# Performance work log

Measured on AMD Instinct MI355X. Metric: run time of the kernel, lower is better.

The kernel has to match this reference:

```python
import jax, jax.numpy as jnp
from jax import lax
import numpy as np

T, B, X, Y = 24, 16, 32, 32
FS, FM, FC = 64, 16, 16
I = FS + FM + FC  # GRU input size = 96
H = 32            # hidden_size


def setup_inputs() -> dict:
    key = jax.random.key(0)
    ks = jax.random.split(key, 8)
    s = 1.0 / np.sqrt(H)  # pytorch GRU init scale
    return {
        "spatial": jax.random.normal(ks[0], (B, X, Y, FS), jnp.float32),
        "meteorology": jax.random.normal(ks[1], (T, B, X, Y, FM), jnp.float32),
        "context": jax.random.normal(ks[2], (T, B, X, Y, FC), jnp.float32),
        "W_ih": jax.random.uniform(ks[3], (3 * H, I), jnp.float32, -s, s),
        "W_hh": jax.random.uniform(ks[4], (3 * H, H), jnp.float32, -s, s),
        "b_ih": jax.random.uniform(ks[5], (3 * H,), jnp.float32, -s, s),
        "b_hh": jax.random.uniform(ks[6], (3 * H,), jnp.float32, -s, s),
        "W": jax.random.normal(ks[7], (H, FS), jnp.float32),
    }


def _gru_final_state(x, W_ih, W_hh, b_ih, b_hh):
    # x: (T, N, I); returns final hidden state (N, H). PyTorch GRU cell math.
    n_batch = x.shape[1]
    h0 = jnp.zeros((n_batch, H), x.dtype)

    def step(h, xt):
        gi = xt @ W_ih.T + b_ih          # (N, 3H)
        gh = h @ W_hh.T + b_hh           # (N, 3H)
        i_r, i_z, i_n = jnp.split(gi, 3, axis=-1)
        h_r, h_z, h_n = jnp.split(gh, 3, axis=-1)
        r = jax.nn.sigmoid(i_r + h_r)
        z = jax.nn.sigmoid(i_z + h_z)
        n = jnp.tanh(i_n + r * h_n)
        h_new = (1.0 - z) * n + z * h
        return h_new, None

    hT, _ = lax.scan(step, h0, x)
    return hT


def reference(spatial, meteorology, context, W_ih, W_hh, b_ih, b_hh, W):
    # Broadcast static spatial features over time and concat along feature dim.
    t = meteorology.shape[0]
    sp = jnp.broadcast_to(spatial[None], (t,) + spatial.shape)
    x = jnp.concatenate([sp, meteorology, context], axis=-1)  # (T,B,X,Y,I)
    # Batch all spatial positions into one recurrence: (T, B*X*Y, I)
    x = x.reshape(t, B * X * Y, I)
    hT = _gru_final_state(x, W_ih, W_hh, b_ih, b_hh)          # (B*X*Y, H)
    out = hT @ W                                              # (B*X*Y, FS)
    return out.reshape(B, X, Y, FS)
```

## Files before the change

kernel.cpp:

```cpp
#include <hip/hip_runtime.h>
#include <hip/hip_fp16.h>
#include <math.h>


typedef __attribute__((ext_vector_type(8))) _Float16 half8;
typedef __attribute__((ext_vector_type(4))) float f32x4;
typedef __attribute__((ext_vector_type(4))) unsigned int uix4;

#define NSEQ 16384
#define TSTEPS 24
#define LOG2E 1.44269504088896340736f

__device__ __forceinline__ float exp2_fast(float x) {
#if __has_builtin(__builtin_amdgcn_exp2f)
  return __builtin_amdgcn_exp2f(x);
#else
  return __expf(x * 0.6931471805599453f);
#endif
}

__device__ __forceinline__ unsigned int pk_f16(float a, float b) {
#if __has_builtin(__builtin_amdgcn_cvt_pkrtz)
  auto r = __builtin_amdgcn_cvt_pkrtz(a, b);
  return __builtin_bit_cast(unsigned int, r);
#else
  return (unsigned)__half_as_ushort(__float2half(a)) |
         ((unsigned)__half_as_ushort(__float2half(b)) << 16);
#endif
}
__device__ __forceinline__ unsigned int pk_f16_rn(float a, float b) {
  return (unsigned)__half_as_ushort(__float2half(a)) |
         ((unsigned)__half_as_ushort(__float2half(b)) << 16);
}
__device__ __forceinline__ half8 mk_h8(unsigned int a, unsigned int b,
                                       unsigned int c, unsigned int d) {
  uix4 v = {a, b, c, d};
  return __builtin_bit_cast(half8, v);
}
__device__ __forceinline__ f32x4 mfma_h(half8 a, half8 b, f32x4 c) {
  return __builtin_amdgcn_mfma_f32_16x16x32_f16(a, b, c, 0, 0, 0);
}

__device__ __forceinline__ void barrier_lds() {
  asm volatile("s_waitcnt lgkmcnt(0)" ::: "memory");
  __builtin_amdgcn_s_barrier();
}

__global__ __launch_bounds__(128, 4)
void gru10(const float* __restrict__ spatial,
           const float* __restrict__ met,
           const float* __restrict__ ctx,
           const float* __restrict__ W_ih,
           const float* __restrict__ W_hh,
           const float* __restrict__ b_ih,
           const float* __restrict__ b_hh,
           const float* __restrict__ Wp,
           float* __restrict__ out) {
  __shared__ float xls[2][6][16][20];

  const int tid = threadIdx.x;
  const int lane = tid & 63;
  const int wv = tid >> 6;
  const int l15 = lane & 15;
  const int c = lane >> 4;
  const int seq = blockIdx.x * 16 + l15;
  const f32x4 zero4 = {0.f, 0.f, 0.f, 0.f};

  if (wv == 1) {
    half8 wmc[6];
    f32x4 acc_i[6];
#pragma unroll
    for (int j = 0; j < 6; ++j) {
      const float sc = (j < 4) ? LOG2E : (2.0f * LOG2E);
      const float* mr = W_ih + (size_t)(j * 16 + l15) * 96 + 64 + c * 8;
      float4 wa = *(const float4*)mr;
      float4 wb = *(const float4*)(mr + 4);
      wmc[j] = mk_h8(pk_f16_rn(wa.x * sc, wa.y * sc),
                     pk_f16_rn(wa.z * sc, wa.w * sc),
                     pk_f16_rn(wb.x * sc, wb.y * sc),
                     pk_f16_rn(wb.z * sc, wb.w * sc));
      const int rowb = j * 16 + 4 * c;
      float4 vih = *(const float4*)(b_ih + rowb);
      if (j < 4) {
        float4 vhh = *(const float4*)(b_hh + rowb);
        acc_i[j][0] = (vih.x + vhh.x) * sc; acc_i[j][1] = (vih.y + vhh.y) * sc;
        acc_i[j][2] = (vih.z + vhh.z) * sc; acc_i[j][3] = (vih.w + vhh.w) * sc;
      } else {
        acc_i[j][0] = vih.x * sc; acc_i[j][1] = vih.y * sc;
        acc_i[j][2] = vih.z * sc; acc_i[j][3] = vih.w * sc;
      }
    }
#pragma unroll
    for (int kt = 0; kt < 2; ++kt) {
      const float* sp = spatial + (size_t)seq * 64 + kt * 32 + c * 8;
      float4 a0 = *(const float4*)sp;
      float4 a1 = *(const float4*)(sp + 4);
      half8 sf = mk_h8(pk_f16(a0.x, a0.y), pk_f16(a0.z, a0.w),
                       pk_f16(a1.x, a1.y), pk_f16(a1.z, a1.w));
#pragma unroll
      for (int j = 0; j < 6; ++j) {
        const float sc = (j < 4) ? LOG2E : (2.0f * LOG2E);
        const float* wr = W_ih + (size_t)(j * 16 + l15) * 96 + kt * 32 + c * 8;
        float4 wa = *(const float4*)wr;
        float4 wb = *(const float4*)(wr + 4);
        half8 wsp = mk_h8(pk_f16_rn(wa.x * sc, wa.y * sc),
                          pk_f16_rn(wa.z * sc, wa.w * sc),
                          pk_f16_rn(wb.x * sc, wb.y * sc),
                          pk_f16_rn(wb.z * sc, wb.w * sc));
        acc_i[j] = mfma_h(wsp, sf, acc_i[j]);
      }
    }
    const float* lptr = ((c < 2) ? met : ctx) + (size_t)seq * 16 + (c & 1) * 8;
    {
      float4 a0 = *(const float4*)lptr;
      float4 a1 = *(const float4*)(lptr + 4);
      half8 xf = mk_h8(pk_f16(a0.x, a0.y), pk_f16(a0.z, a0.w),
                       pk_f16(a1.x, a1.y), pk_f16(a1.z, a1.w));
#pragma unroll
      for (int j = 0; j < 6; ++j) {
        f32x4 D = mfma_h(wmc[j], xf, acc_i[j]);
        *(f32x4*)&xls[0][j][l15][c * 4] = D;
      }
    }
    float4 xs0a = *(const float4*)(lptr + (size_t)1 * NSEQ * 16);
    float4 xs0b = *(const float4*)(lptr + (size_t)1 * NSEQ * 16 + 4);
    float4 xs1a = *(const float4*)(lptr + (size_t)2 * NSEQ * 16);
    float4 xs1b = *(const float4*)(lptr + (size_t)2 * NSEQ * 16 + 4);

    barrier_lds();

#pragma unroll 2
    for (int t = 0; t < TSTEPS; ++t) {
      float4 xa = (t & 1) ? xs1a : xs0a;
      float4 xb = (t & 1) ? xs1b : xs0b;
      half8 xf = mk_h8(pk_f16(xa.x, xa.y), pk_f16(xa.z, xa.w),
                       pk_f16(xb.x, xb.y), pk_f16(xb.z, xb.w));
      {
        int tf = (t + 3 < TSTEPS) ? (t + 3) : (TSTEPS - 1);
        float4 na = *(const float4*)(lptr + (size_t)tf * NSEQ * 16);
        float4 nb = *(const float4*)(lptr + (size_t)tf * NSEQ * 16 + 4);
        if (t & 1) { xs1a = na; xs1b = nb; } else { xs0a = na; xs0b = nb; }
      }
      const int buf = (t + 1) & 1;
#pragma unroll
      for (int j = 0; j < 6; ++j) {
        f32x4 D = mfma_h(wmc[j], xf, acc_i[j]);
        *(f32x4*)&xls[buf][j][l15][c * 4] = D;
      }
      barrier_lds();
    }
  } else {
    __builtin_amdgcn_s_setprio(1);
    half8 whh[6];
#pragma unroll
    for (int j = 0; j < 6; ++j) {
      const float sc = (j < 4) ? LOG2E : (2.0f * LOG2E);
      const float* wr = W_hh + (size_t)(j * 16 + l15) * 32;
      float4 a = *(const float4*)(wr + 4 * c);
      float4 b = *(const float4*)(wr + 16 + 4 * c);
      whh[j] = mk_h8(pk_f16_rn(a.x * sc, a.y * sc),
                     pk_f16_rn(a.z * sc, a.w * sc),
                     pk_f16_rn(b.x * sc, b.y * sc),
                     pk_f16_rn(b.z * sc, b.w * sc));
    }
    f32x4 bhnA, bhnB;
    {
      float4 va = *(const float4*)(b_hh + 64 + 4 * c);
      float4 vb = *(const float4*)(b_hh + 64 + 16 + 4 * c);
      bhnA[0] = 2.0f * LOG2E * va.x; bhnA[1] = 2.0f * LOG2E * va.y;
      bhnA[2] = 2.0f * LOG2E * va.z; bhnA[3] = 2.0f * LOG2E * va.w;
      bhnB[0] = 2.0f * LOG2E * vb.x; bhnB[1] = 2.0f * LOG2E * vb.y;
      bhnB[2] = 2.0f * LOG2E * vb.z; bhnB[3] = 2.0f * LOG2E * vb.w;
    }
    float hst[8];
#pragma unroll
    for (int i = 0; i < 8; ++i) hst[i] = 0.0f;
    half8 fh = mk_h8(0u, 0u, 0u, 0u);

    barrier_lds();

#pragma unroll 2
    for (int t = 0; t < TSTEPS; ++t) {
      const int buf = t & 1;
      f32x4 xr0 = *(const f32x4*)&xls[buf][0][l15][c * 4];
      f32x4 xr1 = *(const f32x4*)&xls[buf][1][l15][c * 4];
      f32x4 xz0 = *(const f32x4*)&xls[buf][2][l15][c * 4];
      f32x4 xz1 = *(const f32x4*)&xls[buf][3][l15][c * 4];
      f32x4 ti0 = *(const f32x4*)&xls[buf][4][l15][c * 4];
      f32x4 ti1 = *(const f32x4*)&xls[buf][5][l15][c * 4];

      f32x4 dr0 = mfma_h(whh[0], fh, xr0);
      f32x4 dr1 = mfma_h(whh[1], fh, xr1);
      f32x4 dz0 = mfma_h(whh[2], fh, xz0);
      f32x4 dz1 = mfma_h(whh[3], fh, xz1);
      f32x4 th0 = mfma_h(whh[4], fh, bhnA);
      f32x4 th1 = mfma_h(whh[5], fh, bhnB);

      float hv_[8];
#pragma unroll
      for (int jj = 0; jj < 2; ++jj) {
        f32x4 ddr = jj ? dr1 : dr0;
        f32x4 ddz = jj ? dz1 : dz0;
        f32x4 tth = jj ? th1 : th0;
        f32x4 tti = jj ? ti1 : ti0;
#pragma unroll
        for (int q = 0; q < 4; ++q) {
          const int i = jj * 4 + q;
          float R = exp2_fast(-ddr[q]);
          float r = __builtin_amdgcn_rcpf(1.0f + R);
          float E = fminf(exp2_fast(-ddz[q]), 1e30f);
          float Y = fmaf(r, tth[q], tti[q]);
          float e = fminf(exp2_fast(-Y), 1e30f);
          float oe = 1.0f + e, oE = 1.0f + E;
          float inv = __builtin_amdgcn_rcpf(oE * oe);
          float num = fmaf(hst[i], oe, fmaf(-E, e, E));
          float hv = num * inv;
          hst[i] = hv;
          hv_[i] = hv;
        }
      }
      fh = mk_h8(pk_f16(hv_[0], hv_[1]), pk_f16(hv_[2], hv_[3]),
                 pk_f16(hv_[4], hv_[5]), pk_f16(hv_[6], hv_[7]));

      barrier_lds();
    }

#pragma unroll
    for (int pt = 0; pt < 4; ++pt) {
      const int frow = pt * 16 + l15;
      const float* wpb = Wp + frow;
      float v[8];
#pragma unroll
      for (int e = 0; e < 8; ++e) {
        int col = (e < 4) ? (4 * c + e) : (16 + 4 * c + (e - 4));
        v[e] = wpb[(size_t)col * 64];
      }
      unsigned int uh[4], ul[4];
#pragma unroll
      for (int e2 = 0; e2 < 4; ++e2) {
        float va = v[2 * e2], vb = v[2 * e2 + 1];
        __half ha = __float2half(va), hb = __float2half(vb);
        float la = va - __half2float(ha), lb = vb - __half2float(hb);
        uh[e2] = (unsigned)__half_as_ushort(ha) |
                 ((unsigned)__half_as_ushort(hb) << 16);
        ul[e2] = pk_f16_rn(la, lb);
      }
      half8 wph = mk_h8(uh[0], uh[1], uh[2], uh[3]);
      half8 wpl = mk_h8(ul[0], ul[1], ul[2], ul[3]);
      f32x4 o = mfma_h(wph, fh, zero4);
      o = mfma_h(wpl, fh, o);
      float* op = out + (size_t)seq * 64 + pt * 16 + 4 * c;
      *(float4*)op = make_float4(o[0], o[1], o[2], o[3]);
    }
    __builtin_amdgcn_s_setprio(0);
  }
}

extern "C" void kernel_launch(void* const* d_in, const int* in_sizes, int n_in,
                              void* d_out, int out_size, void* d_ws, size_t ws_size,
                              hipStream_t stream) {
  const float* spatial = (const float*)d_in[0];
  const float* met     = (const float*)d_in[1];
  const float* ctx     = (const float*)d_in[2];
  const float* W_ih    = (const float*)d_in[3];
  const float* W_hh    = (const float*)d_in[4];
  const float* b_ih    = (const float*)d_in[5];
  const float* b_hh    = (const float*)d_in[6];
  const float* Wp      = (const float*)d_in[7];
  float* out = (float*)d_out;

  hipLaunchKernelGGL(gru10, dim3(1024), dim3(128), 0, stream,
                     spatial, met, ctx, W_ih, W_hh, b_ih, b_hh, Wp, out);
}
```

Baseline: 23.69 us.

## Batch two timesteps per producer-consumer handoff to halve barriers

The input-projection wave now computes two timesteps of gate pre-activations per LDS buffer, so the recurrence wave syncs once every two steps instead of every step. The LDS buffer doubles to hold two steps per slot, and global prefetch is reorganised to keep two step-pairs in flight. This cuts barrier count from 24 to 12 and lets the consumer issue all twelve LDS reads up front, at the cost of more registers and LDS per block, which could reduce occupancy.

```diff
diff --git a/kernel.cpp b/kernel.cpp
--- a/kernel.cpp
+++ b/kernel.cpp
@@ -9,6 +9,7 @@
 
 #define NSEQ 16384
 #define TSTEPS 24
+#define NINT 12
 #define LOG2E 1.44269504088896340736f
 
 __device__ __forceinline__ float exp2_fast(float x) {
@@ -47,7 +48,7 @@
 }
 
 __global__ __launch_bounds__(128, 4)
-void gru10(const float* __restrict__ spatial,
+void gru11(const float* __restrict__ spatial,
            const float* __restrict__ met,
            const float* __restrict__ ctx,
            const float* __restrict__ W_ih,
@@ -56,7 +57,7 @@
            const float* __restrict__ b_hh,
            const float* __restrict__ Wp,
            float* __restrict__ out) {
-  __shared__ float xls[2][6][16][20];
+  __shared__ float xls[2][2][6][16][20];
 
   const int tid = threadIdx.x;
   const int lane = tid & 63;
@@ -111,43 +112,41 @@
       }
     }
     const float* lptr = ((c < 2) ? met : ctx) + (size_t)seq * 16 + (c & 1) * 8;
-    {
-      float4 a0 = *(const float4*)lptr;
-      float4 a1 = *(const float4*)(lptr + 4);
-      half8 xf = mk_h8(pk_f16(a0.x, a0.y), pk_f16(a0.z, a0.w),
-                       pk_f16(a1.x, a1.y), pk_f16(a1.z, a1.w));
+
+    auto fill = [&](int buf, int s, float4 xa, float4 xb) {
+      half8 xf = mk_h8(pk_f16(xa.x, xa.y), pk_f16(xa.z, xa.w),
+                       pk_f16(xb.x, xb.y), pk_f16(xb.z, xb.w));
 #pragma unroll
       for (int j = 0; j < 6; ++j) {
         f32x4 D = mfma_h(wmc[j], xf, acc_i[j]);
-        *(f32x4*)&xls[0][j][l15][c * 4] = D;
-      }
-    }
-    float4 xs0a = *(const float4*)(lptr + (size_t)1 * NSEQ * 16);
-    float4 xs0b = *(const float4*)(lptr + (size_t)1 * NSEQ * 16 + 4);
-    float4 xs1a = *(const float4*)(lptr + (size_t)2 * NSEQ * 16);
-    float4 xs1b = *(const float4*)(lptr + (size_t)2 * NSEQ * 16 + 4);
-
-    barrier_lds();
+        *(f32x4*)&xls[buf][s][j][l15][c * 4] = D;
+      }
+    };
+    auto ldx = [&](int t, float4& a, float4& b) {
+      const float* p = lptr + (size_t)t * NSEQ * 16;
+      a = *(const float4*)p; b = *(const float4*)(p + 4);
+    };
+
+    {
+      float4 a0, b0, a1, b1;
+      ldx(0, a0, b0); ldx(1, a1, b1);
+      fill(0, 0, a0, b0); fill(0, 1, a1, b1);
+    }
+    float4 c0a, c0b, c1a, c1b, n0a, n0b, n1a, n1b;
+    ldx(2, c0a, c0b); ldx(3, c1a, c1b);
+    ldx(4, n0a, n0b); ldx(5, n1a, n1b);
 
 #pragma unroll 2
-    for (int t = 0; t < TSTEPS; ++t) {
-      float4 xa = (t & 1) ? xs1a : xs0a;
-      float4 xb = (t & 1) ? xs1b : xs0b;
-      half8 xf = mk_h8(pk_f16(xa.x, xa.y), pk_f16(xa.z, xa.w),
-                       pk_f16(xb.x, xb.y), pk_f16(xb.z, xb.w));
-      {
-        int tf = (t + 3 < TSTEPS) ? (t + 3) : (TSTEPS - 1);
-        float4 na = *(const float4*)(lptr + (size_t)tf * NSEQ * 16);
-        float4 nb = *(const float4*)(lptr + (size_t)tf * NSEQ * 16 + 4);
-        if (t & 1) { xs1a = na; xs1b = nb; } else { xs0a = na; xs0b = nb; }
-      }
-      const int buf = (t + 1) & 1;
-#pragma unroll
-      for (int j = 0; j < 6; ++j) {
-        f32x4 D = mfma_h(wmc[j], xf, acc_i[j]);
-        *(f32x4*)&xls[buf][j][l15][c * 4] = D;
-      }
+    for (int k = 0; k < NINT; ++k) {
       barrier_lds();
+      if (k < NINT - 1) {
+        fill((k + 1) & 1, 0, c0a, c0b);
+        fill((k + 1) & 1, 1, c1a, c1b);
+        c0a = n0a; c0b = n0b; c1a = n1a; c1b = n1b;
+        int t0 = (2 * k + 6 < TSTEPS) ? (2 * k + 6) : (TSTEPS - 1);
+        int t1 = (2 * k + 7 < TSTEPS) ? (2 * k + 7) : (TSTEPS - 1);
+        ldx(t0, n0a, n0b); ldx(t1, n1a, n1b);
+      }
     }
   } else {
     __builtin_amdgcn_s_setprio(1);
@@ -177,25 +176,14 @@
     for (int i = 0; i < 8; ++i) hst[i] = 0.0f;
     half8 fh = mk_h8(0u, 0u, 0u, 0u);
 
-    barrier_lds();
-
-#pragma unroll 2
-    for (int t = 0; t < TSTEPS; ++t) {
-      const int buf = t & 1;
-      f32x4 xr0 = *(const f32x4*)&xls[buf][0][l15][c * 4];
-      f32x4 xr1 = *(const f32x4*)&xls[buf][1][l15][c * 4];
-      f32x4 xz0 = *(const f32x4*)&xls[buf][2][l15][c * 4];
-      f32x4 xz1 = *(const f32x4*)&xls[buf][3][l15][c * 4];
-      f32x4 ti0 = *(const f32x4*)&xls[buf][4][l15][c * 4];
-      f32x4 ti1 = *(const f32x4*)&xls[buf][5][l15][c * 4];
-
+    auto do_step = [&](f32x4 xr0, f32x4 xr1, f32x4 xz0, f32x4 xz1,
+                       f32x4 ti0, f32x4 ti1) {
       f32x4 dr0 = mfma_h(whh[0], fh, xr0);
       f32x4 dr1 = mfma_h(whh[1], fh, xr1);
       f32x4 dz0 = mfma_h(whh[2], fh, xz0);
       f32x4 dz1 = mfma_h(whh[3], fh, xz1);
       f32x4 th0 = mfma_h(whh[4], fh, bhnA);
       f32x4 th1 = mfma_h(whh[5], fh, bhnB);
-
       float hv_[8];
 #pragma unroll
       for (int jj = 0; jj < 2; ++jj) {
@@ -221,8 +209,26 @@
       }
       fh = mk_h8(pk_f16(hv_[0], hv_[1]), pk_f16(hv_[2], hv_[3]),
                  pk_f16(hv_[4], hv_[5]), pk_f16(hv_[6], hv_[7]));
-
+    };
+
+#pragma unroll 2
+    for (int k = 0; k < NINT; ++k) {
+      const int buf = k & 1;
       barrier_lds();
+      f32x4 A0 = *(const f32x4*)&xls[buf][0][0][l15][c * 4];
+      f32x4 A1 = *(const f32x4*)&xls[buf][0][1][l15][c * 4];
+      f32x4 A2 = *(const f32x4*)&xls[buf][0][2][l15][c * 4];
+      f32x4 A3 = *(const f32x4*)&xls[buf][0][3][l15][c * 4];
+      f32x4 A4 = *(const f32x4*)&xls[buf][0][4][l15][c * 4];
+      f32x4 A5 = *(const f32x4*)&xls[buf][0][5][l15][c * 4];
+      f32x4 B0 = *(const f32x4*)&xls[buf][1][0][l15][c * 4];
+      f32x4 B1 = *(const f32x4*)&xls[buf][1][1][l15][c * 4];
+      f32x4 B2 = *(const f32x4*)&xls[buf][1][2][l15][c * 4];
+      f32x4 B3 = *(const f32x4*)&xls[buf][1][3][l15][c * 4];
+      f32x4 B4 = *(const f32x4*)&xls[buf][1][4][l15][c * 4];
+      f32x4 B5 = *(const f32x4*)&xls[buf][1][5][l15][c * 4];
+      do_step(A0, A1, A2, A3, A4, A5);
+      do_step(B0, B1, B2, B3, B4, B5);
     }
 
 #pragma unroll
@@ -269,6 +275,6 @@
   const float* Wp      = (const float*)d_in[7];
   float* out = (float*)d_out;
 
-  hipLaunchKernelGGL(gru10, dim3(1024), dim3(128), 0, stream,
+  hipLaunchKernelGGL(gru11, dim3(1024), dim3(128), 0, stream,
                      spatial, met, ctx, W_ih, W_hh, b_ih, b_hh, Wp, out);
 }
```

Result: slower. 25.04 us (+5.7%).

## Process two 16-sequence groups per block to interleave independent GRU recurrences

Applied to the files above, without the earlier changes.

Each block now handles 32 sequences as two independent 16-sequence groups, so grid size halves and both the input-projection wave and the recurrence wave interleave two independent chains. The intent is to hide MFMA and transcendental latency in the serial per-step dependency via instruction-level parallelism and to amortize barriers and weight setup across twice the work. It costs doubled registers and LDS per block, fewer blocks (512 vs 1024 on the device's CUs), and the launch-bounds occupancy hint is dropped.

```diff
diff --git a/kernel.cpp b/kernel.cpp
--- a/kernel.cpp
+++ b/kernel.cpp
@@ -46,8 +46,8 @@
   __builtin_amdgcn_s_barrier();
 }
 
-__global__ __launch_bounds__(128, 4)
-void gru10(const float* __restrict__ spatial,
+__global__ __launch_bounds__(128)
+void gru13(const float* __restrict__ spatial,
            const float* __restrict__ met,
            const float* __restrict__ ctx,
            const float* __restrict__ W_ih,
@@ -56,19 +56,20 @@
            const float* __restrict__ b_hh,
            const float* __restrict__ Wp,
            float* __restrict__ out) {
-  __shared__ float xls[2][6][16][20];
+  __shared__ float xls[2][2][6][16][20];
 
   const int tid = threadIdx.x;
   const int lane = tid & 63;
   const int wv = tid >> 6;
   const int l15 = lane & 15;
   const int c = lane >> 4;
-  const int seq = blockIdx.x * 16 + l15;
+  const int seq0 = blockIdx.x * 32 + l15;
+  const int seq1 = seq0 + 16;
   const f32x4 zero4 = {0.f, 0.f, 0.f, 0.f};
 
   if (wv == 1) {
     half8 wmc[6];
-    f32x4 acc_i[6];
+    f32x4 acc_i[2][6];
 #pragma unroll
     for (int j = 0; j < 6; ++j) {
       const float sc = (j < 4) ? LOG2E : (2.0f * LOG2E);
@@ -81,71 +82,102 @@
                      pk_f16_rn(wb.z * sc, wb.w * sc));
       const int rowb = j * 16 + 4 * c;
       float4 vih = *(const float4*)(b_ih + rowb);
+      float bv0, bv1, bv2, bv3;
       if (j < 4) {
         float4 vhh = *(const float4*)(b_hh + rowb);
-        acc_i[j][0] = (vih.x + vhh.x) * sc; acc_i[j][1] = (vih.y + vhh.y) * sc;
-        acc_i[j][2] = (vih.z + vhh.z) * sc; acc_i[j][3] = (vih.w + vhh.w) * sc;
+        bv0 = (vih.x + vhh.x) * sc; bv1 = (vih.y + vhh.y) * sc;
+        bv2 = (vih.z + vhh.z) * sc; bv3 = (vih.w + vhh.w) * sc;
       } else {
-        acc_i[j][0] = vih.x * sc; acc_i[j][1] = vih.y * sc;
-        acc_i[j][2] = vih.z * sc; acc_i[j][3] = vih.w * sc;
-      }
-    }
-#pragma unroll
-    for (int kt = 0; kt < 2; ++kt) {
-      const float* sp = spatial + (size_t)seq * 64 + kt * 32 + c * 8;
-      float4 a0 = *(const float4*)sp;
-      float4 a1 = *(const float4*)(sp + 4);
-      half8 sf = mk_h8(pk_f16(a0.x, a0.y), pk_f16(a0.z, a0.w),
-                       pk_f16(a1.x, a1.y), pk_f16(a1.z, a1.w));
-#pragma unroll
-      for (int j = 0; j < 6; ++j) {
-        const float sc = (j < 4) ? LOG2E : (2.0f * LOG2E);
-        const float* wr = W_ih + (size_t)(j * 16 + l15) * 96 + kt * 32 + c * 8;
-        float4 wa = *(const float4*)wr;
-        float4 wb = *(const float4*)(wr + 4);
-        half8 wsp = mk_h8(pk_f16_rn(wa.x * sc, wa.y * sc),
-                          pk_f16_rn(wa.z * sc, wa.w * sc),
-                          pk_f16_rn(wb.x * sc, wb.y * sc),
-                          pk_f16_rn(wb.z * sc, wb.w * sc));
-        acc_i[j] = mfma_h(wsp, sf, acc_i[j]);
-      }
-    }
-    const float* lptr = ((c < 2) ? met : ctx) + (size_t)seq * 16 + (c & 1) * 8;
-    {
-      float4 a0 = *(const float4*)lptr;
-      float4 a1 = *(const float4*)(lptr + 4);
+        bv0 = vih.x * sc; bv1 = vih.y * sc; bv2 = vih.z * sc; bv3 = vih.w * sc;
+      }
+#pragma unroll
+      for (int g = 0; g < 2; ++g) {
+        acc_i[g][j][0] = bv0; acc_i[g][j][1] = bv1;
+        acc_i[g][j][2] = bv2; acc_i[g][j][3] = bv3;
+      }
+    }
+#pragma unroll
+    for (int g = 0; g < 2; ++g) {
+      const int seqg = g ? seq1 : seq0;
+#pragma unroll
+      for (int kt = 0; kt < 2; ++kt) {
+        const float* sp = spatial + (size_t)seqg * 64 + kt * 32 + c * 8;
+        float4 a0 = *(const float4*)sp;
+        float4 a1 = *(const float4*)(sp + 4);
+        half8 sf = mk_h8(pk_f16(a0.x, a0.y), pk_f16(a0.z, a0.w),
+                         pk_f16(a1.x, a1.y), pk_f16(a1.z, a1.w));
+#pragma unroll
+        for (int j = 0; j < 6; ++j) {
+          const float sc = (j < 4) ? LOG2E : (2.0f * LOG2E);
+          const float* wr = W_ih + (size_t)(j * 16 + l15) * 96 + kt * 32 + c * 8;
+          float4 wa = *(const float4*)wr;
+          float4 wb = *(const float4*)(wr + 4);
+          half8 wsp = mk_h8(pk_f16_rn(wa.x * sc, wa.y * sc),
+                            pk_f16_rn(wa.z * sc, wa.w * sc),
+                            pk_f16_rn(wb.x * sc, wb.y * sc),
+                            pk_f16_rn(wb.z * sc, wb.w * sc));
+          acc_i[g][j] = mfma_h(wsp, sf, acc_i[g][j]);
+        }
+      }
+    }
+    const float* lp0 = ((c < 2) ? met : ctx) + (size_t)seq0 * 16 + (c & 1) * 8;
+    const float* lp1 = ((c < 2) ? met : ctx) + (size_t)seq1 * 16 + (c & 1) * 8;
+
+#pragma unroll
+    for (int g = 0; g < 2; ++g) {
+      const float* lp = g ? lp1 : lp0;
+      float4 a0 = *(const float4*)lp;
+      float4 a1 = *(const float4*)(lp + 4);
       half8 xf = mk_h8(pk_f16(a0.x, a0.y), pk_f16(a0.z, a0.w),
                        pk_f16(a1.x, a1.y), pk_f16(a1.z, a1.w));
 #pragma unroll
       for (int j = 0; j < 6; ++j) {
-        f32x4 D = mfma_h(wmc[j], xf, acc_i[j]);
-        *(f32x4*)&xls[0][j][l15][c * 4] = D;
-      }
-    }
-    float4 xs0a = *(const float4*)(lptr + (size_t)1 * NSEQ * 16);
-    float4 xs0b = *(const float4*)(lptr + (size_t)1 * NSEQ * 16 + 4);
-    float4 xs1a = *(const float4*)(lptr + (size_t)2 * NSEQ * 16);
-    float4 xs1b = *(const float4*)(lptr + (size_t)2 * NSEQ * 16 + 4);
+        f32x4 D = mfma_h(wmc[j], xf, acc_i[g][j]);
+        *(f32x4*)&xls[0][g][j][l15][c * 4] = D;
+      }
+    }
+    float4 s00a = *(const float4*)(lp0 + (size_t)1 * NSEQ * 16);
+    float4 s00b = *(const float4*)(lp0 + (size_t)1 * NSEQ * 16 + 4);
+    float4 s01a = *(const float4*)(lp0 + (size_t)2 * NSEQ * 16);
+    float4 s01b = *(const float4*)(lp0 + (size_t)2 * NSEQ * 16 + 4);
+    float4 s10a = *(const float4*)(lp1 + (size_t)1 * NSEQ * 16);
+    float4 s10b = *(const float4*)(lp1 + (size_t)1 * NSEQ * 16 + 4);
+    float4 s11a = *(const float4*)(lp1 + (size_t)2 * NSEQ * 16);
+    float4 s11b = *(const float4*)(lp1 + (size_t)2 * NSEQ * 16 + 4);
 
     barrier_lds();
 
 #pragma unroll 2
     for (int t = 0; t < TSTEPS; ++t) {
-      float4 xa = (t & 1) ? xs1a : xs0a;
-      float4 xb = (t & 1) ? xs1b : xs0b;
-      half8 xf = mk_h8(pk_f16(xa.x, xa.y), pk_f16(xa.z, xa.w),
-                       pk_f16(xb.x, xb.y), pk_f16(xb.z, xb.w));
+      const int buf = (t + 1) & 1;
+      const int tf = (t + 3 < TSTEPS) ? (t + 3) : (TSTEPS - 1);
       {
-        int tf = (t + 3 < TSTEPS) ? (t + 3) : (TSTEPS - 1);
-        float4 na = *(const float4*)(lptr + (size_t)tf * NSEQ * 16);
-        float4 nb = *(const float4*)(lptr + (size_t)tf * NSEQ * 16 + 4);
-        if (t & 1) { xs1a = na; xs1b = nb; } else { xs0a = na; xs0b = nb; }
-      }
-      const int buf = (t + 1) & 1;
-#pragma unroll
-      for (int j = 0; j < 6; ++j) {
-        f32x4 D = mfma_h(wmc[j], xf, acc_i[j]);
-        *(f32x4*)&xls[buf][j][l15][c * 4] = D;
+        float4 xa = (t & 1) ? s01a : s00a;
+        float4 xb = (t & 1) ? s01b : s00b;
+        half8 xf = mk_h8(pk_f16(xa.x, xa.y), pk_f16(xa.z, xa.w),
+                         pk_f16(xb.x, xb.y), pk_f16(xb.z, xb.w));
+#pragma unroll
+        for (int j = 0; j < 6; ++j) {
+          f32x4 D = mfma_h(wmc[j], xf, acc_i[0][j]);
+          *(f32x4*)&xls[buf][0][j][l15][c * 4] = D;
+        }
+        float4 na = *(const float4*)(lp0 + (size_t)tf * NSEQ * 16);
+        float4 nb = *(const float4*)(lp0 + (size_t)tf * NSEQ * 16 + 4);
+        if (t & 1) { s01a = na; s01b = nb; } else { s00a = na; s00b = nb; }
+      }
+      {
+        float4 xa = (t & 1) ? s11a : s10a;
+        float4 xb = (t & 1) ? s11b : s10b;
+        half8 xf = mk_h8(pk_f16(xa.x, xa.y), pk_f16(xa.z, xa.w),
+                         pk_f16(xb.x, xb.y), pk_f16(xb.z, xb.w));
+#pragma unroll
+        for (int j = 0; j < 6; ++j) {
+          f32x4 D = mfma_h(wmc[j], xf, acc_i[1][j]);
+          *(f32x4*)&xls[buf][1][j][l15][c * 4] = D;
+        }
+        float4 na = *(const float4*)(lp1 + (size_t)tf * NSEQ * 16);
+        float4 nb = *(const float4*)(lp1 + (size_t)tf * NSEQ * 16 + 4);
+        if (t & 1) { s11a = na; s11b = nb; } else { s10a = na; s10b = nb; }
       }
       barrier_lds();
     }
@@ -172,55 +204,83 @@
       bhnB[0] = 2.0f * LOG2E * vb.x; bhnB[1] = 2.0f * LOG2E * vb.y;
       bhnB[2] = 2.0f * LOG2E * vb.z; bhnB[3] = 2.0f * LOG2E * vb.w;
     }
-    float hst[8];
-#pragma unroll
-    for (int i = 0; i < 8; ++i) hst[i] = 0.0f;
-    half8 fh = mk_h8(0u, 0u, 0u, 0u);
+    float hstA[8], hstB[8];
+#pragma unroll
+    for (int i = 0; i < 8; ++i) { hstA[i] = 0.0f; hstB[i] = 0.0f; }
+    half8 fhA = mk_h8(0u, 0u, 0u, 0u);
+    half8 fhB = mk_h8(0u, 0u, 0u, 0u);
 
     barrier_lds();
 
 #pragma unroll 2
     for (int t = 0; t < TSTEPS; ++t) {
       const int buf = t & 1;
-      f32x4 xr0 = *(const f32x4*)&xls[buf][0][l15][c * 4];
-      f32x4 xr1 = *(const f32x4*)&xls[buf][1][l15][c * 4];
-      f32x4 xz0 = *(const f32x4*)&xls[buf][2][l15][c * 4];
-      f32x4 xz1 = *(const f32x4*)&xls[buf][3][l15][c * 4];
-      f32x4 ti0 = *(const f32x4*)&xls[buf][4][l15][c * 4];
-      f32x4 ti1 = *(const f32x4*)&xls[buf][5][l15][c * 4];
-
-      f32x4 dr0 = mfma_h(whh[0], fh, xr0);
-      f32x4 dr1 = mfma_h(whh[1], fh, xr1);
-      f32x4 dz0 = mfma_h(whh[2], fh, xz0);
-      f32x4 dz1 = mfma_h(whh[3], fh, xz1);
-      f32x4 th0 = mfma_h(whh[4], fh, bhnA);
-      f32x4 th1 = mfma_h(whh[5], fh, bhnB);
-
-      float hv_[8];
+      f32x4 a0 = *(const f32x4*)&xls[buf][0][0][l15][c * 4];
+      f32x4 a1 = *(const f32x4*)&xls[buf][0][1][l15][c * 4];
+      f32x4 a2 = *(const f32x4*)&xls[buf][0][2][l15][c * 4];
+      f32x4 a3 = *(const f32x4*)&xls[buf][0][3][l15][c * 4];
+      f32x4 a4 = *(const f32x4*)&xls[buf][0][4][l15][c * 4];
+      f32x4 a5 = *(const f32x4*)&xls[buf][0][5][l15][c * 4];
+      f32x4 b0 = *(const f32x4*)&xls[buf][1][0][l15][c * 4];
+      f32x4 b1 = *(const f32x4*)&xls[buf][1][1][l15][c * 4];
+      f32x4 b2 = *(const f32x4*)&xls[buf][1][2][l15][c * 4];
+      f32x4 b3 = *(const f32x4*)&xls[buf][1][3][l15][c * 4];
+      f32x4 b4 = *(const f32x4*)&xls[buf][1][4][l15][c * 4];
+      f32x4 b5 = *(const f32x4*)&xls[buf][1][5][l15][c * 4];
+
+      f32x4 Adr0 = mfma_h(whh[0], fhA, a0);
+      f32x4 Bdr0 = mfma_h(whh[0], fhB, b0);
+      f32x4 Adr1 = mfma_h(whh[1], fhA, a1);
+      f32x4 Bdr1 = mfma_h(whh[1], fhB, b1);
+      f32x4 Adz0 = mfma_h(whh[2], fhA, a2);
+      f32x4 Bdz0 = mfma_h(whh[2], fhB, b2);
+      f32x4 Adz1 = mfma_h(whh[3], fhA, a3);
+      f32x4 Bdz1 = mfma_h(whh[3], fhB, b3);
+      f32x4 Ath0 = mfma_h(whh[4], fhA, bhnA);
+      f32x4 Bth0 = mfma_h(whh[4], fhB, bhnA);
+      f32x4 Ath1 = mfma_h(whh[5], fhA, bhnB);
+      f32x4 Bth1 = mfma_h(whh[5], fhB, bhnB);
+
+      float hvA[8], hvB[8];
 #pragma unroll
       for (int jj = 0; jj < 2; ++jj) {
-        f32x4 ddr = jj ? dr1 : dr0;
-        f32x4 ddz = jj ? dz1 : dz0;
-        f32x4 tth = jj ? th1 : th0;
-        f32x4 tti = jj ? ti1 : ti0;
+        f32x4 Addr = jj ? Adr1 : Adr0;  f32x4 Bddr = jj ? Bdr1 : Bdr0;
+        f32x4 Addz = jj ? Adz1 : Adz0;  f32x4 Bddz = jj ? Bdz1 : Bdz0;
+        f32x4 Atth = jj ? Ath1 : Ath0;  f32x4 Btth = jj ? Bth1 : Bth0;
+        f32x4 Atti = jj ? a5 : a4;      f32x4 Btti = jj ? b5 : b4;
 #pragma unroll
         for (int q = 0; q < 4; ++q) {
           const int i = jj * 4 + q;
-          float R = exp2_fast(-ddr[q]);
-          float r = __builtin_amdgcn_rcpf(1.0f + R);
-          float E = fminf(exp2_fast(-ddz[q]), 1e30f);
-          float Y = fmaf(r, tth[q], tti[q]);
-          float e = fminf(exp2_fast(-Y), 1e30f);
-          float oe = 1.0f + e, oE = 1.0f + E;
-          float inv = __builtin_amdgcn_rcpf(oE * oe);
-          float num = fmaf(hst[i], oe, fmaf(-E, e, E));
-          float hv = num * inv;
-          hst[i] = hv;
-          hv_[i] = hv;
+          {
+            float R = exp2_fast(-Addr[q]);
+            float r = __builtin_amdgcn_rcpf(1.0f + R);
+            float E = fminf(exp2_fast(-Addz[q]), 1e30f);
+            float Y = fmaf(r, Atth[q], Atti[q]);
+            float e = fminf(exp2_fast(-Y), 1e30f);
+            float oe = 1.0f + e, oE = 1.0f + E;
+            float inv = __builtin_amdgcn_rcpf(oE * oe);
+            float num = fmaf(hstA[i], oe, fmaf(-E, e, E));
+            float hv = num * inv;
+            hstA[i] = hv; hvA[i] = hv;
+          }
+          {
+            float R = exp2_fast(-Bddr[q]);
+            float r = __builtin_amdgcn_rcpf(1.0f + R);
+            float E = fminf(exp2_fast(-Bddz[q]), 1e30f);
+            float Y = fmaf(r, Btth[q], Btti[q]);
+            float e = fminf(exp2_fast(-Y), 1e30f);
+            float oe = 1.0f + e, oE = 1.0f + E;
+            float inv = __builtin_amdgcn_rcpf(oE * oe);
+            float num = fmaf(hstB[i], oe, fmaf(-E, e, E));
+            float hv = num * inv;
+            hstB[i] = hv; hvB[i] = hv;
+          }
         }
       }
-      fh = mk_h8(pk_f16(hv_[0], hv_[1]), pk_f16(hv_[2], hv_[3]),
-                 pk_f16(hv_[4], hv_[5]), pk_f16(hv_[6], hv_[7]));
+      fhA = mk_h8(pk_f16(hvA[0], hvA[1]), pk_f16(hvA[2], hvA[3]),
+                  pk_f16(hvA[4], hvA[5]), pk_f16(hvA[6], hvA[7]));
+      fhB = mk_h8(pk_f16(hvB[0], hvB[1]), pk_f16(hvB[2], hvB[3]),
+                  pk_f16(hvB[4], hvB[5]), pk_f16(hvB[6], hvB[7]));
 
       barrier_lds();
     }
@@ -247,10 +307,14 @@
       }
       half8 wph = mk_h8(uh[0], uh[1], uh[2], uh[3]);
       half8 wpl = mk_h8(ul[0], ul[1], ul[2], ul[3]);
-      f32x4 o = mfma_h(wph, fh, zero4);
-      o = mfma_h(wpl, fh, o);
-      float* op = out + (size_t)seq * 64 + pt * 16 + 4 * c;
-      *(float4*)op = make_float4(o[0], o[1], o[2], o[3]);
+      f32x4 oA = mfma_h(wph, fhA, zero4);
+      oA = mfma_h(wpl, fhA, oA);
+      f32x4 oB = mfma_h(wph, fhB, zero4);
+      oB = mfma_h(wpl, fhB, oB);
+      float* opA = out + (size_t)seq0 * 64 + pt * 16 + 4 * c;
+      *(float4*)opA = make_float4(oA[0], oA[1], oA[2], oA[3]);
+      float* opB = out + (size_t)seq1 * 64 + pt * 16 + 4 * c;
+      *(float4*)opB = make_float4(oB[0], oB[1], oB[2], oB[3]);
     }
     __builtin_amdgcn_s_setprio(0);
   }
@@ -269,6 +333,6 @@
   const float* Wp      = (const float*)d_in[7];
   float* out = (float*)d_out;
 
-  hipLaunchKernelGGL(gru10, dim3(1024), dim3(128), 0, stream,
+  hipLaunchKernelGGL(gru13, dim3(512), dim3(128), 0, stream,
                      spatial, met, ctx, W_ih, W_hh, b_ih, b_hh, Wp, out);
 }
```

Result: slower. 37.31 us (+57.5%).
